# Performance work log

Measured on AMD Instinct MI355X. Metric: run time of the kernel, lower is better.

The kernel has to match this reference:

```python
import jax, jax.numpy as jnp
import numpy as np

EMBED = 1024
HEADS = 16
HEAD_DIM = 64
FF = 4096
EPS = 1e-5


def _layernorm(x, g, b):
    mu = jnp.mean(x, axis=-1, keepdims=True)
    var = jnp.mean(jnp.square(x - mu), axis=-1, keepdims=True)
    return (x - mu) * jax.lax.rsqrt(var + EPS) * g + b


def setup_inputs() -> dict:
    key = jax.random.key(0)
    ks = jax.random.split(key, 12)
    s_in = 1.0 / np.sqrt(EMBED)
    s_hd = 1.0 / np.sqrt(HEADS * HEAD_DIM)
    s_ff = 1.0 / np.sqrt(FF)
    return {
        "x": jax.random.normal(ks[0], (4, 2048, EMBED), dtype=jnp.float32),
        "Wq": jax.random.uniform(ks[1], (HEADS, EMBED, HEAD_DIM), jnp.float32, -s_in, s_in),
        "Wk": jax.random.uniform(ks[2], (HEADS, EMBED, HEAD_DIM), jnp.float32, -s_in, s_in),
        "Wv": jax.random.uniform(ks[3], (HEADS, EMBED, HEAD_DIM), jnp.float32, -s_in, s_in),
        "Wo": jax.random.uniform(ks[4], (HEADS * HEAD_DIM, EMBED), jnp.float32, -s_hd, s_hd),
        "bo": jax.random.uniform(ks[5], (EMBED,), jnp.float32, -s_hd, s_hd),
        "W1": jax.random.uniform(ks[6], (EMBED, FF), jnp.float32, -s_in, s_in),
        "b1": jax.random.uniform(ks[7], (FF,), jnp.float32, -s_in, s_in),
        "W2": jax.random.uniform(ks[8], (FF, EMBED), jnp.float32, -s_ff, s_ff),
        "b2": jax.random.uniform(ks[9], (EMBED,), jnp.float32, -s_ff, s_ff),
        "ln1_g": jnp.ones((EMBED,), jnp.float32),
        "ln1_b": jnp.zeros((EMBED,), jnp.float32),
        "ln2_g": jnp.ones((EMBED,), jnp.float32),
        "ln2_b": jnp.zeros((EMBED,), jnp.float32),
    }


def reference(x, Wq, Wk, Wv, Wo, bo, W1, b1, W2, b2, ln1_g, ln1_b, ln2_g, ln2_b):
    B, T, C = x.shape
    h = _layernorm(x, ln1_g, ln1_b)
    # per-head projections, batched over heads: [B,H,T,Dh]
    q = jnp.einsum("btc,hcd->bhtd", h, Wq)
    k = jnp.einsum("btc,hcd->bhtd", h, Wk)
    v = jnp.einsum("btc,hcd->bhtd", h, Wv)
    scale = HEAD_DIM ** -0.5
    att = jnp.einsum("bhtd,bhsd->bhts", q, k) * scale  # [B,H,T,T]
    causal = jnp.tril(jnp.ones((T, T), dtype=bool))
    att = jnp.where(causal, att, -jnp.inf)
    att = jax.nn.softmax(att, axis=-1)
    out = jnp.einsum("bhts,bhsd->bhtd", att, v)  # [B,H,T,Dh]
    # concat heads (matches torch.cat over head outputs) -> [B,T,H*Dh]
    out = out.transpose(0, 2, 1, 3).reshape(B, T, HEADS * HEAD_DIM)
    x = x + out @ Wo + bo
    h2 = _layernorm(x, ln2_g, ln2_b)
    ff = jax.nn.relu(h2 @ W1 + b1) @ W2 + b2
    return x + ff
```

## Files before the change

kernel.cpp:

```cpp
#include <hip/hip_runtime.h>
#include <hip/hip_bf16.h>

#define EMBED 1024
#define HEADS 16
#define HEAD_DIM 64
#define FFDIM 4096
#define TSEQ 2048
#define BATCH 4
#define ROWS (BATCH * TSEQ)

typedef __bf16 bf16;
typedef __attribute__((ext_vector_type(8))) __bf16 bf16x8;
typedef __attribute__((ext_vector_type(4))) __bf16 bf16x4;
typedef __attribute__((ext_vector_type(4))) float f32x4;
typedef __attribute__((ext_vector_type(16))) float f32x16;
typedef __attribute__((ext_vector_type(2))) unsigned u32x2;

typedef const __attribute__((address_space(1))) void* gvp;
typedef __attribute__((address_space(3))) void* svp;

__device__ inline unsigned pk2(float a, float b) {
  union { bf16 h[2]; unsigned u; } x;
  x.h[0] = (bf16)a;
  x.h[1] = (bf16)b;
  return x.u;
}

__global__ __launch_bounds__(256) void conv_wqkv_t(
    const float* __restrict__ Wq, const float* __restrict__ Wk,
    const float* __restrict__ Wv, bf16* __restrict__ WqkvT) {
  __shared__ bf16 t[64][72];
  int tid = threadIdx.x;
  int k0 = blockIdx.x * 64;
  int head = blockIdx.y;
  int which = blockIdx.z;
  const float* src = which == 0 ? Wq : which == 1 ? Wk : Wv;
  float scale = which == 0 ? 0.125f * 1.44269504088896f : 1.0f;
  src += (size_t)head * 65536;
  bf16* dst = WqkvT + ((size_t)which * 1024 + head * 64) * 1024;
#pragma unroll
  for (int i = 0; i < 4; ++i) {
    int r = i * 16 + (tid >> 4);
    int c = (tid & 15) * 4;
    float4 v = *(const float4*)&src[(size_t)(k0 + r) * 64 + c];
    t[c + 0][r] = (bf16)(v.x * scale);
    t[c + 1][r] = (bf16)(v.y * scale);
    t[c + 2][r] = (bf16)(v.z * scale);
    t[c + 3][r] = (bf16)(v.w * scale);
  }
  __syncthreads();
#pragma unroll
  for (int i = 0; i < 2; ++i) {
    int r = i * 32 + (tid >> 3);
    int c = (tid & 7) * 8;
    bf16x8 o;
#pragma unroll
    for (int j = 0; j < 8; ++j) o[j] = t[r][c + j];
    *(bf16x8*)&dst[(size_t)r * 1024 + k0 + c] = o;
  }
}

__global__ __launch_bounds__(256) void transpose_conv(
    const float* __restrict__ W, bf16* __restrict__ WT, int K, int N) {
  __shared__ bf16 t[64][72];
  int tid = threadIdx.x;
  int n0 = blockIdx.x * 64, k0 = blockIdx.y * 64;
#pragma unroll
  for (int i = 0; i < 4; ++i) {
    int r = i * 16 + (tid >> 4);
    int c = (tid & 15) * 4;
    float4 v = *(const float4*)&W[(size_t)(k0 + r) * N + n0 + c];
    t[c + 0][r] = (bf16)v.x;
    t[c + 1][r] = (bf16)v.y;
    t[c + 2][r] = (bf16)v.z;
    t[c + 3][r] = (bf16)v.w;
  }
  __syncthreads();
#pragma unroll
  for (int i = 0; i < 2; ++i) {
    int r = i * 32 + (tid >> 3);
    int c = (tid & 7) * 8;
    bf16x8 o;
#pragma unroll
    for (int j = 0; j < 8; ++j) o[j] = t[r][c + j];
    *(bf16x8*)&WT[(size_t)(n0 + r) * K + k0 + c] = o;
  }
}

__global__ __launch_bounds__(256) void transpose_v(const bf16* __restrict__ v,
                                                   bf16* __restrict__ vt) {
  __shared__ bf16 t[64][72];
  int bh = blockIdx.y;
  int t0 = blockIdx.x * 64;
  const bf16* src = v + (size_t)bh * 131072;
  bf16* dst = vt + (size_t)bh * 131072;
  int tid = threadIdx.x;
#pragma unroll
  for (int i = 0; i < 2; ++i) {
    int c = tid + i * 256;
    int r = c >> 3, d0 = (c & 7) * 8;
    bf16x8 vv = *(const bf16x8*)&src[(size_t)(t0 + r) * 64 + d0];
#pragma unroll
    for (int j = 0; j < 8; ++j) t[d0 + j][r] = vv[j];
  }
  __syncthreads();
#pragma unroll
  for (int i = 0; i < 2; ++i) {
    int c = tid + i * 256;
    int r = c >> 3, s0 = (c & 7) * 8;
    bf16x8 o;
#pragma unroll
    for (int j = 0; j < 8; ++j) o[j] = t[r][s0 + j];
    *(bf16x8*)&dst[(size_t)r * 2048 + t0 + s0] = o;
  }
}

__global__ __launch_bounds__(256) void ln_kernel(
    const float* __restrict__ x, const float* __restrict__ g,
    const float* __restrict__ bta, bf16* __restrict__ out) {
  int row = blockIdx.x;
  const float* xr = x + (size_t)row * EMBED;
  float4 v = ((const float4*)xr)[threadIdx.x];
  float s1 = v.x + v.y + v.z + v.w;
  float s2 = v.x * v.x + v.y * v.y + v.z * v.z + v.w * v.w;
#pragma unroll
  for (int off = 1; off < 64; off <<= 1) {
    s1 += __shfl_xor(s1, off);
    s2 += __shfl_xor(s2, off);
  }
  __shared__ float red[8];
  int wid = threadIdx.x >> 6;
  int lane = threadIdx.x & 63;
  if (lane == 0) {
    red[wid * 2] = s1;
    red[wid * 2 + 1] = s2;
  }
  __syncthreads();
  s1 = red[0] + red[2] + red[4] + red[6];
  s2 = red[1] + red[3] + red[5] + red[7];
  float mu = s1 * (1.0f / EMBED);
  float var = s2 * (1.0f / EMBED) - mu * mu;
  float rs = rsqrtf(var + 1e-5f);
  float4 gv = ((const float4*)g)[threadIdx.x];
  float4 bv = ((const float4*)bta)[threadIdx.x];
  bf16x4 o;
  o[0] = (bf16)((v.x - mu) * rs * gv.x + bv.x);
  o[1] = (bf16)((v.y - mu) * rs * gv.y + bv.y);
  o[2] = (bf16)((v.z - mu) * rs * gv.z + bv.z);
  o[3] = (bf16)((v.w - mu) * rs * gv.w + bv.w);
  *(bf16x4*)(out + (size_t)row * EMBED + threadIdx.x * 4) = o;
}

template <int EPI>
__global__ __launch_bounds__(512, 1) void gemm256(
    const bf16* __restrict__ A, const bf16* __restrict__ BT,
    bf16* __restrict__ Cb, const float* __restrict__ bias, int M, int N,
    int K) {
  __shared__ __attribute__((aligned(16))) char lds[98304];
  int gx = gridDim.x;
  int nwg = gx * gridDim.y;
  int wgid = blockIdx.y * gx + blockIdx.x;
  int cpx = nwg >> 3;
  int swz = (wgid & 7) * cpx + (wgid >> 3);
  int m0 = (swz / gx) * 256, n0 = (swz % gx) * 256;
  int tid = threadIdx.x;
  int lane = tid & 63, wid = tid >> 6;
  int lr = lane & 15, lg = lane >> 4;
  int wrM = (wid >> 2) * 128;
  int wcN = (wid & 3) * 64;
  int crow = lane >> 2;
  int slotg = (lane & 3) ^ ((crow >> 1) & 3);
  int NT = K >> 5;
  size_t rb = (size_t)K * 2;

  auto stageA = [&](int t) {
    char* dst = lds + ((unsigned)t % 3u) * 32768u;
#pragma unroll
    for (int q = 0; q < 2; ++q) {
      int c = wid * 2 + q;
      const char* srcA = (const char*)A + (size_t)(m0 + c * 16 + crow) * rb +
                         (size_t)t * 64 + slotg * 16;
      __builtin_amdgcn_global_load_lds((gvp)srcA, (svp)(dst + c * 1024), 16, 0,
                                       0);
    }
  };
  auto stageB = [&](int t) {
    char* dst = lds + ((unsigned)t % 3u) * 32768u + 16384u;
#pragma unroll
    for (int q = 0; q < 2; ++q) {
      int c = wid * 2 + q;
      const char* srcB = (const char*)BT + (size_t)(n0 + c * 16 + crow) * rb +
                         (size_t)t * 64 + slotg * 16;
      __builtin_amdgcn_global_load_lds((gvp)srcB, (svp)(dst + c * 1024), 16, 0,
                                       0);
    }
  };

  stageA(0);
  stageB(0);
  stageA(1);
  stageB(1);
  f32x4 acc[8][4] = {};
  int swcol = ((lg ^ ((lr >> 1) & 3)) * 16);
  for (int t = 0; t < NT; ++t) {
    if (t == NT - 1)
      asm volatile("s_waitcnt vmcnt(0)" ::: "memory");
    else
      asm volatile("s_waitcnt vmcnt(4)" ::: "memory");
    __builtin_amdgcn_s_barrier();
    __builtin_amdgcn_sched_barrier(0);
    const char* Ab = lds + ((unsigned)t % 3u) * 32768u;
    const char* Bb = Ab + 16384;
    int tn = t + 2;
    bool st = tn < NT;
    bf16x8 bfr[4], afA[4], afB[4];
#pragma unroll
    for (int j = 0; j < 4; ++j)
      bfr[j] = *(const bf16x8*)(Bb + (wcN + j * 16 + lr) * 64 + swcol);
#pragma unroll
    for (int i = 0; i < 4; ++i)
      afA[i] = *(const bf16x8*)(Ab + (wrM + i * 16 + lr) * 64 + swcol);
    if (st) stageA(tn);
    __builtin_amdgcn_s_barrier();
    __builtin_amdgcn_sched_barrier(0);
    __builtin_amdgcn_s_setprio(1);
#pragma unroll
    for (int i = 0; i < 4; ++i)
#pragma unroll
      for (int j = 0; j < 4; ++j)
        acc[i][j] = __builtin_amdgcn_mfma_f32_16x16x32_bf16(afA[i], bfr[j],
                                                            acc[i][j], 0, 0, 0);
    __builtin_amdgcn_s_setprio(0);
    __builtin_amdgcn_sched_barrier(0);
#pragma unroll
    for (int i = 0; i < 4; ++i)
      afB[i] = *(const bf16x8*)(Ab + (wrM + 64 + i * 16 + lr) * 64 + swcol);
    if (st) stageB(tn);
    __builtin_amdgcn_s_barrier();
    __builtin_amdgcn_sched_barrier(0);
    __builtin_amdgcn_s_setprio(1);
#pragma unroll
    for (int i = 0; i < 4; ++i)
#pragma unroll
      for (int j = 0; j < 4; ++j)
        acc[4 + i][j] = __builtin_amdgcn_mfma_f32_16x16x32_bf16(
            afB[i], bfr[j], acc[4 + i][j], 0, 0, 0);
    __builtin_amdgcn_s_setprio(0);
    __builtin_amdgcn_sched_barrier(0);
  }
#pragma unroll
  for (int i = 0; i < 8; ++i) {
#pragma unroll
    for (int j = 0; j < 4; ++j) {
#pragma unroll
      for (int r = 0; r < 4; ++r) {
        int row = m0 + wrM + i * 16 + lg * 4 + r;
        int col = n0 + wcN + j * 16 + lr;
        float v = acc[i][j][r];
        if (EPI == 0) {
          int which = col >> 10, cc = col & 1023;
          int b = row >> 11, tt = row & 2047, h = cc >> 6, d = cc & 63;
          bf16* dst = Cb + (size_t)which * 8388608;
          dst[((size_t)((b << 4) + h) * TSEQ + tt) * HEAD_DIM + d] = (bf16)v;
        } else {
          size_t o = (size_t)row * N + col;
          float u = v + bias[col];
          Cb[o] = (bf16)(u > 0.f ? u : 0.f);
        }
      }
    }
  }
}

__global__ __launch_bounds__(512, 2) void gemm_res(
    const bf16* __restrict__ A, const bf16* __restrict__ BT,
    float* __restrict__ Cf, const float* __restrict__ bias,
    const float* __restrict__ resid, int M, int N, int K) {
  __shared__ __attribute__((aligned(16))) char lds[73728];
  int gx = gridDim.x;
  int nwg = gx * gridDim.y;
  int wgid = blockIdx.y * gx + blockIdx.x;
  int cpx = nwg >> 3;
  int swz = (wgid & 7) * cpx + (wgid >> 3);
  int m0 = (swz / gx) * 256, n0 = (swz % gx) * 128;
  int tid = threadIdx.x;
  int lane = tid & 63, wid = tid >> 6;
  int lr = lane & 15, lg = lane >> 4;
  int wrM = (wid >> 1) * 64;
  int wcN = (wid & 1) * 64;
  int crow = lane >> 2;
  int slotg = (lane & 3) ^ ((crow >> 1) & 3);
  int NT = K >> 5;
  size_t rb = (size_t)K * 2;

  auto stageA = [&](int t) {
    char* dst = lds + ((unsigned)t % 3u) * 24576u;
#pragma unroll
    for (int q = 0; q < 2; ++q) {
      int c = wid * 2 + q;
      const char* srcA = (const char*)A + (size_t)(m0 + c * 16 + crow) * rb +
                         (size_t)t * 64 + slotg * 16;
      __builtin_amdgcn_global_load_lds((gvp)srcA, (svp)(dst + c * 1024), 16, 0,
                                       0);
    }
  };
  auto stageB = [&](int t) {
    char* dst = lds + ((unsigned)t % 3u) * 24576u + 16384u;
    const char* srcB = (const char*)BT + (size_t)(n0 + wid * 16 + crow) * rb +
                       (size_t)t * 64 + slotg * 16;
    __builtin_amdgcn_global_load_lds((gvp)srcB, (svp)(dst + wid * 1024), 16, 0,
                                     0);
  };

  stageA(0);
  stageB(0);
  stageA(1);
  stageB(1);
  f32x4 acc[4][4] = {};
  int swcol = ((lg ^ ((lr >> 1) & 3)) * 16);
  for (int t = 0; t < NT; ++t) {
    if (t == NT - 1)
      asm volatile("s_waitcnt vmcnt(0)" ::: "memory");
    else
      asm volatile("s_waitcnt vmcnt(3)" ::: "memory");
    __builtin_amdgcn_s_barrier();
    __builtin_amdgcn_sched_barrier(0);
    const char* Ab = lds + ((unsigned)t % 3u) * 24576u;
    const char* Bb = Ab + 16384;
    int tn = t + 2;
    bool st = tn < NT;
    bf16x8 bfr[4], afA[2], afB[2];
#pragma unroll
    for (int j = 0; j < 4; ++j)
      bfr[j] = *(const bf16x8*)(Bb + (wcN + j * 16 + lr) * 64 + swcol);
#pragma unroll
    for (int i = 0; i < 2; ++i)
      afA[i] = *(const bf16x8*)(Ab + (wrM + i * 16 + lr) * 64 + swcol);
    if (st) stageA(tn);
    __builtin_amdgcn_s_barrier();
    __builtin_amdgcn_sched_barrier(0);
    __builtin_amdgcn_s_setprio(1);
#pragma unroll
    for (int i = 0; i < 2; ++i)
#pragma unroll
      for (int j = 0; j < 4; ++j)
        acc[i][j] = __builtin_amdgcn_mfma_f32_16x16x32_bf16(afA[i], bfr[j],
                                                            acc[i][j], 0, 0, 0);
    __builtin_amdgcn_s_setprio(0);
    __builtin_amdgcn_sched_barrier(0);
#pragma unroll
    for (int i = 0; i < 2; ++i)
      afB[i] = *(const bf16x8*)(Ab + (wrM + 32 + i * 16 + lr) * 64 + swcol);
    if (st) stageB(tn);
    __builtin_amdgcn_s_barrier();
    __builtin_amdgcn_sched_barrier(0);
    __builtin_amdgcn_s_setprio(1);
#pragma unroll
    for (int i = 0; i < 2; ++i)
#pragma unroll
      for (int j = 0; j < 4; ++j)
        acc[2 + i][j] = __builtin_amdgcn_mfma_f32_16x16x32_bf16(
            afB[i], bfr[j], acc[2 + i][j], 0, 0, 0);
    __builtin_amdgcn_s_setprio(0);
    __builtin_amdgcn_sched_barrier(0);
  }
#pragma unroll
  for (int i = 0; i < 4; ++i) {
#pragma unroll
    for (int j = 0; j < 4; ++j) {
#pragma unroll
      for (int r = 0; r < 4; ++r) {
        int row = m0 + wrM + i * 16 + lg * 4 + r;
        int col = n0 + wcN + j * 16 + lr;
        size_t o = (size_t)row * N + col;
        Cf[o] = resid[o] + bias[col] + acc[i][j][r];
      }
    }
  }
}

__global__ __launch_bounds__(256) void attn_kernel(
    const bf16* __restrict__ q, const bf16* __restrict__ k,
    const bf16* __restrict__ vt, bf16* __restrict__ out) {
  __shared__ __attribute__((aligned(16))) char ldsK[8192];
  __shared__ __attribute__((aligned(16))) char ldsV[8192];
  int bh = blockIdx.x;
  int b = bh >> 4, h = bh & 15;
  const bf16* qb = q + (size_t)bh * TSEQ * HEAD_DIM;
  const bf16* kb = k + (size_t)bh * TSEQ * HEAD_DIM;
  const bf16* vb = vt + (size_t)bh * HEAD_DIM * TSEQ;
  int tid = threadIdx.x, lane = tid & 63, w = tid >> 6;
  int l31 = lane & 31, hi = lane >> 5;
  int Q = 15 - blockIdx.y;
  int tw = Q * 128 + w * 32;
  int qrow = tw + l31;
  int srow0 = tid >> 3;
  int scol = (tid & 7) * 16;
  int swz31 = (l31 & 7) << 4;
  bf16x8 aq[4];
#pragma unroll
  for (int f = 0; f < 4; ++f)
    aq[f] = *(const bf16x8*)&qb[(size_t)qrow * HEAD_DIM + f * 16 + hi * 8];
  f32x16 o0 = {}, o1 = {};
  f32x16 minit;
#pragma unroll
  for (int i = 0; i < 16; ++i) minit[i] = -8.0f;
  float sacc = 0.f;
  int nj = 2 * Q + 2;
  for (int j = 0; j < nj; ++j) {
#pragma unroll
    for (int i = 0; i < 2; ++i) {
      int rr = srow0 + i * 32;
      int sw = scol ^ ((rr & 7) << 4);
      *(bf16x8*)(ldsK + rr * 128 + sw) =
          *(const bf16x8*)&kb[(size_t)(j * 64 + rr) * HEAD_DIM + (scol >> 1)];
      *(bf16x8*)(ldsV + rr * 128 + sw) =
          *(const bf16x8*)&vb[(size_t)rr * TSEQ + j * 64 + (scol >> 1)];
    }
    __syncthreads();
    if (j * 64 <= tw + 31) {
      f32x16 s0 = minit, s1 = minit;
#pragma unroll
      for (int f = 0; f < 4; ++f) {
        int colb = (f * 32 + hi * 16) ^ swz31;
        bf16x8 ka = *(const bf16x8*)(ldsK + l31 * 128 + colb);
        bf16x8 kb2 = *(const bf16x8*)(ldsK + (32 + l31) * 128 + colb);
        s0 = __builtin_amdgcn_mfma_f32_32x32x16_bf16(ka, aq[f], s0, 0, 0, 0);
        s1 = __builtin_amdgcn_mfma_f32_32x32x16_bf16(kb2, aq[f], s1, 0, 0, 0);
      }
      if (j >= 2 * Q) {
#pragma unroll
        for (int reg = 0; reg < 16; ++reg) {
          int key = j * 64 + (reg & 3) + 8 * (reg >> 2) + 4 * hi;
          if (key > qrow) s0[reg] = -1e30f;
          if (key + 32 > qrow) s1[reg] = -1e30f;
        }
      }
      unsigned pk0[8], pk1[8];
#pragma unroll
      for (int p = 0; p < 8; ++p) {
        float a0 = exp2f(s0[2 * p]), b0 = exp2f(s0[2 * p + 1]);
        float a1 = exp2f(s1[2 * p]), b1 = exp2f(s1[2 * p + 1]);
        sacc += (a0 + b0) + (a1 + b1);
        pk0[p] = pk2(a0, b0);
        pk1[p] = pk2(a1, b1);
      }
#pragma unroll
      for (int ks = 0; ks < 4; ++ks) {
        const unsigned* P = (ks >> 1) ? pk1 : pk0;
        int kp = (ks & 1) * 4;
        union { unsigned u[4]; bf16x8 v; } pa;
#if __has_builtin(__builtin_amdgcn_permlane32_swap)
        u32x2 r02 = __builtin_amdgcn_permlane32_swap(P[kp + 0], P[kp + 2],
                                                     false, false);
        u32x2 r13 = __builtin_amdgcn_permlane32_swap(P[kp + 1], P[kp + 3],
                                                     false, false);
        pa.u[0] = r02.x;
        pa.u[2] = r02.y;
        pa.u[1] = r13.x;
        pa.u[3] = r13.y;
#else
        unsigned x0 = P[kp + 0], x1 = P[kp + 1];
        unsigned x2 = P[kp + 2], x3 = P[kp + 3];
        unsigned y0 = (unsigned)__shfl_xor((int)x0, 32);
        unsigned y1 = (unsigned)__shfl_xor((int)x1, 32);
        unsigned y2 = (unsigned)__shfl_xor((int)x2, 32);
        unsigned y3 = (unsigned)__shfl_xor((int)x3, 32);
        pa.u[0] = hi ? y2 : x0;
        pa.u[1] = hi ? y3 : x1;
        pa.u[2] = hi ? x2 : y0;
        pa.u[3] = hi ? x3 : y1;
#endif
        int colb = (ks * 32 + hi * 16) ^ swz31;
        bf16x8 bv0 = *(const bf16x8*)(ldsV + l31 * 128 + colb);
        bf16x8 bv1 = *(const bf16x8*)(ldsV + (32 + l31) * 128 + colb);
        o0 = __builtin_amdgcn_mfma_f32_32x32x16_bf16(pa.v, bv0, o0, 0, 0, 0);
        o1 = __builtin_amdgcn_mfma_f32_32x32x16_bf16(pa.v, bv1, o1, 0, 0, 0);
      }
    }
    __syncthreads();
  }
  float tot = sacc + __shfl_xor(sacc, 32);
#pragma unroll
  for (int reg = 0; reg < 16; ++reg) {
    int ql = (reg & 3) + 8 * (reg >> 2) + 4 * hi;
    float lw = __shfl(tot, ql);
    float rl = 1.0f / lw;
    int t = tw + ql;
    size_t o = ((size_t)(b * TSEQ) + t) * EMBED + h * HEAD_DIM;
    out[o + l31] = (bf16)(o0[reg] * rl);
    out[o + 32 + l31] = (bf16)(o1[reg] * rl);
  }
}

extern "C" void kernel_launch(void* const* d_in, const int* in_sizes, int n_in,
                              void* d_out, int out_size, void* d_ws,
                              size_t ws_size, hipStream_t stream) {
  const float* x = (const float*)d_in[0];
  const float* Wq = (const float*)d_in[1];
  const float* Wk = (const float*)d_in[2];
  const float* Wv = (const float*)d_in[3];
  const float* Wo = (const float*)d_in[4];
  const float* bo = (const float*)d_in[5];
  const float* W1 = (const float*)d_in[6];
  const float* b1 = (const float*)d_in[7];
  const float* W2 = (const float*)d_in[8];
  const float* b2 = (const float*)d_in[9];
  const float* g1 = (const float*)d_in[10];
  const float* be1 = (const float*)d_in[11];
  const float* g2 = (const float*)d_in[12];
  const float* be2 = (const float*)d_in[13];
  float* out = (float*)d_out;
  char* ws = (char*)d_ws;

  const size_t U = 16777216;
  bf16* h = (bf16*)(ws + 0 * U);
  bf16* qb = (bf16*)(ws + 1 * U);
  bf16* vtb = (bf16*)(ws + 0 * U);
  bf16* vnb = (bf16*)(ws + 3 * U);
  bf16* ao = (bf16*)(ws + 3 * U);
  float* x1 = (float*)(ws + 4 * U);
  bf16* h2 = (bf16*)(ws + 6 * U);
  bf16* ff1 = (bf16*)(ws + 0 * U);
  char* wbase = ws + 7 * U;
  bf16* WqkvT = (bf16*)(wbase);
  bf16* WoT = (bf16*)(wbase + 6291456);
  bf16* W1T = (bf16*)(wbase + 8388608);
  bf16* W2T = (bf16*)(wbase + 16777216);

  hipLaunchKernelGGL(conv_wqkv_t, dim3(16, 16, 3), dim3(256), 0, stream, Wq,
                     Wk, Wv, WqkvT);
  hipLaunchKernelGGL(transpose_conv, dim3(16, 16), dim3(256), 0, stream, Wo,
                     WoT, 1024, 1024);
  hipLaunchKernelGGL(transpose_conv, dim3(64, 16), dim3(256), 0, stream, W1,
                     W1T, 1024, 4096);
  hipLaunchKernelGGL(transpose_conv, dim3(16, 64), dim3(256), 0, stream, W2,
                     W2T, 4096, 1024);
  hipLaunchKernelGGL(ln_kernel, dim3(8192), dim3(256), 0, stream, x, g1, be1,
                     h);
  hipLaunchKernelGGL((gemm256<0>), dim3(12, 32), dim3(512), 0, stream, h,
                     WqkvT, qb, (const float*)nullptr, ROWS, 3072, 1024);
  hipLaunchKernelGGL(transpose_v, dim3(32, 64), dim3(256), 0, stream, vnb,
                     vtb);
  hipLaunchKernelGGL(attn_kernel, dim3(64, 16), dim3(256), 0, stream, qb,
                     qb + 8388608, vtb, ao);
  hipLaunchKernelGGL(gemm_res, dim3(8, 32), dim3(512), 0, stream, ao, WoT, x1,
                     bo, x, ROWS, 1024, 1024);
  hipLaunchKernelGGL(ln_kernel, dim3(8192), dim3(256), 0, stream, x1, g2, be2,
                     h2);
  hipLaunchKernelGGL((gemm256<3>), dim3(16, 32), dim3(512), 0, stream, h2, W1T,
                     ff1, b1, ROWS, 4096, 1024);
  hipLaunchKernelGGL(gemm_res, dim3(8, 32), dim3(512), 0, stream, ff1, W2T,
                     out, b2, x1, ROWS, 1024, 4096);
}
```

Before: 382.1 us.

## Shrink attention blocks to 64 queries to drop masked-tile waste

```diff
diff --git a/kernel.cpp b/kernel.cpp
--- a/kernel.cpp
+++ b/kernel.cpp
@@ -14,7 +14,6 @@
 typedef __attribute__((ext_vector_type(4))) __bf16 bf16x4;
 typedef __attribute__((ext_vector_type(4))) float f32x4;
 typedef __attribute__((ext_vector_type(16))) float f32x16;
-typedef __attribute__((ext_vector_type(2))) unsigned u32x2;
 
 typedef const __attribute__((address_space(1))) void* gvp;
 typedef __attribute__((address_space(3))) void* svp;
@@ -379,7 +378,7 @@
   }
 }
 
-__global__ __launch_bounds__(256) void attn_kernel(
+__global__ __launch_bounds__(128) void attn_kernel(
     const bf16* __restrict__ q, const bf16* __restrict__ k,
     const bf16* __restrict__ vt, bf16* __restrict__ out) {
   __shared__ __attribute__((aligned(16))) char ldsK[8192];
@@ -391,8 +390,8 @@
   const bf16* vb = vt + (size_t)bh * HEAD_DIM * TSEQ;
   int tid = threadIdx.x, lane = tid & 63, w = tid >> 6;
   int l31 = lane & 31, hi = lane >> 5;
-  int Q = 15 - blockIdx.y;
-  int tw = Q * 128 + w * 32;
+  int Q = 31 - blockIdx.y;
+  int tw = Q * 64 + w * 32;
   int qrow = tw + l31;
   int srow0 = tid >> 3;
   int scol = (tid & 7) * 16;
@@ -406,11 +405,11 @@
 #pragma unroll
   for (int i = 0; i < 16; ++i) minit[i] = -8.0f;
   float sacc = 0.f;
-  int nj = 2 * Q + 2;
+  int nj = Q + 1;
   for (int j = 0; j < nj; ++j) {
 #pragma unroll
-    for (int i = 0; i < 2; ++i) {
-      int rr = srow0 + i * 32;
+    for (int i = 0; i < 4; ++i) {
+      int rr = srow0 + i * 16;
       int sw = scol ^ ((rr & 7) << 4);
       *(bf16x8*)(ldsK + rr * 128 + sw) =
           *(const bf16x8*)&kb[(size_t)(j * 64 + rr) * HEAD_DIM + (scol >> 1)];
@@ -418,66 +417,55 @@
           *(const bf16x8*)&vb[(size_t)rr * TSEQ + j * 64 + (scol >> 1)];
     }
     __syncthreads();
-    if (j * 64 <= tw + 31) {
-      f32x16 s0 = minit, s1 = minit;
-#pragma unroll
-      for (int f = 0; f < 4; ++f) {
-        int colb = (f * 32 + hi * 16) ^ swz31;
-        bf16x8 ka = *(const bf16x8*)(ldsK + l31 * 128 + colb);
-        bf16x8 kb2 = *(const bf16x8*)(ldsK + (32 + l31) * 128 + colb);
-        s0 = __builtin_amdgcn_mfma_f32_32x32x16_bf16(ka, aq[f], s0, 0, 0, 0);
-        s1 = __builtin_amdgcn_mfma_f32_32x32x16_bf16(kb2, aq[f], s1, 0, 0, 0);
+    f32x16 s0 = minit, s1 = minit;
+    __builtin_amdgcn_s_setprio(1);
+#pragma unroll
+    for (int f = 0; f < 4; ++f) {
+      int colb = (f * 32 + hi * 16) ^ swz31;
+      bf16x8 ka = *(const bf16x8*)(ldsK + l31 * 128 + colb);
+      bf16x8 kb2 = *(const bf16x8*)(ldsK + (32 + l31) * 128 + colb);
+      s0 = __builtin_amdgcn_mfma_f32_32x32x16_bf16(ka, aq[f], s0, 0, 0, 0);
+      s1 = __builtin_amdgcn_mfma_f32_32x32x16_bf16(kb2, aq[f], s1, 0, 0, 0);
+    }
+    __builtin_amdgcn_s_setprio(0);
+    if (j == Q) {
+#pragma unroll
+      for (int reg = 0; reg < 16; ++reg) {
+        int key = j * 64 + (reg & 3) + 8 * (reg >> 2) + 4 * hi;
+        if (key > qrow) s0[reg] = -1e30f;
+        if (key + 32 > qrow) s1[reg] = -1e30f;
       }
-      if (j >= 2 * Q) {
-#pragma unroll
-        for (int reg = 0; reg < 16; ++reg) {
-          int key = j * 64 + (reg & 3) + 8 * (reg >> 2) + 4 * hi;
-          if (key > qrow) s0[reg] = -1e30f;
-          if (key + 32 > qrow) s1[reg] = -1e30f;
-        }
-      }
-      unsigned pk0[8], pk1[8];
-#pragma unroll
-      for (int p = 0; p < 8; ++p) {
-        float a0 = exp2f(s0[2 * p]), b0 = exp2f(s0[2 * p + 1]);
-        float a1 = exp2f(s1[2 * p]), b1 = exp2f(s1[2 * p + 1]);
-        sacc += (a0 + b0) + (a1 + b1);
-        pk0[p] = pk2(a0, b0);
-        pk1[p] = pk2(a1, b1);
-      }
-#pragma unroll
-      for (int ks = 0; ks < 4; ++ks) {
-        const unsigned* P = (ks >> 1) ? pk1 : pk0;
-        int kp = (ks & 1) * 4;
-        union { unsigned u[4]; bf16x8 v; } pa;
-#if __has_builtin(__builtin_amdgcn_permlane32_swap)
-        u32x2 r02 = __builtin_amdgcn_permlane32_swap(P[kp + 0], P[kp + 2],
-                                                     false, false);
-        u32x2 r13 = __builtin_amdgcn_permlane32_swap(P[kp + 1], P[kp + 3],
-                                                     false, false);
-        pa.u[0] = r02.x;
-        pa.u[2] = r02.y;
-        pa.u[1] = r13.x;
-        pa.u[3] = r13.y;
-#else
-        unsigned x0 = P[kp + 0], x1 = P[kp + 1];
-        unsigned x2 = P[kp + 2], x3 = P[kp + 3];
-        unsigned y0 = (unsigned)__shfl_xor((int)x0, 32);
-        unsigned y1 = (unsigned)__shfl_xor((int)x1, 32);
-        unsigned y2 = (unsigned)__shfl_xor((int)x2, 32);
-        unsigned y3 = (unsigned)__shfl_xor((int)x3, 32);
-        pa.u[0] = hi ? y2 : x0;
-        pa.u[1] = hi ? y3 : x1;
-        pa.u[2] = hi ? x2 : y0;
-        pa.u[3] = hi ? x3 : y1;
-#endif
-        int colb = (ks * 32 + hi * 16) ^ swz31;
-        bf16x8 bv0 = *(const bf16x8*)(ldsV + l31 * 128 + colb);
-        bf16x8 bv1 = *(const bf16x8*)(ldsV + (32 + l31) * 128 + colb);
-        o0 = __builtin_amdgcn_mfma_f32_32x32x16_bf16(pa.v, bv0, o0, 0, 0, 0);
-        o1 = __builtin_amdgcn_mfma_f32_32x32x16_bf16(pa.v, bv1, o1, 0, 0, 0);
-      }
-    }
+    }
+    unsigned pk0[8], pk1[8];
+#pragma unroll
+    for (int p = 0; p < 8; ++p) {
+      float a0 = exp2f(s0[2 * p]), b0 = exp2f(s0[2 * p + 1]);
+      float a1 = exp2f(s1[2 * p]), b1 = exp2f(s1[2 * p + 1]);
+      sacc += (a0 + b0) + (a1 + b1);
+      pk0[p] = pk2(a0, b0);
+      pk1[p] = pk2(a1, b1);
+    }
+    __builtin_amdgcn_s_setprio(1);
+#pragma unroll
+    for (int ks = 0; ks < 4; ++ks) {
+      const unsigned* P = (ks >> 1) ? pk1 : pk0;
+      int kp = (ks & 1) * 4;
+      unsigned x0 = P[kp + 0], x1 = P[kp + 1];
+      unsigned x2 = P[kp + 2], x3 = P[kp + 3];
+      asm("v_permlane32_swap_b32 %0, %1" : "+v"(x0), "+v"(x2));
+      asm("v_permlane32_swap_b32 %0, %1" : "+v"(x1), "+v"(x3));
+      union { unsigned u[4]; bf16x8 v; } pa;
+      pa.u[0] = x0;
+      pa.u[1] = x1;
+      pa.u[2] = x2;
+      pa.u[3] = x3;
+      int colb = (ks * 32 + hi * 16) ^ swz31;
+      bf16x8 bv0 = *(const bf16x8*)(ldsV + l31 * 128 + colb);
+      bf16x8 bv1 = *(const bf16x8*)(ldsV + (32 + l31) * 128 + colb);
+      o0 = __builtin_amdgcn_mfma_f32_32x32x16_bf16(pa.v, bv0, o0, 0, 0, 0);
+      o1 = __builtin_amdgcn_mfma_f32_32x32x16_bf16(pa.v, bv1, o1, 0, 0, 0);
+    }
+    __builtin_amdgcn_s_setprio(0);
     __syncthreads();
   }
   float tot = sacc + __shfl_xor(sacc, 32);
@@ -542,7 +530,7 @@
                      WqkvT, qb, (const float*)nullptr, ROWS, 3072, 1024);
   hipLaunchKernelGGL(transpose_v, dim3(32, 64), dim3(256), 0, stream, vnb,
                      vtb);
-  hipLaunchKernelGGL(attn_kernel, dim3(64, 16), dim3(256), 0, stream, qb,
+  hipLaunchKernelGGL(attn_kernel, dim3(64, 32), dim3(128), 0, stream, qb,
                      qb + 8388608, vtb, ao);
   hipLaunchKernelGGL(gemm_res, dim3(8, 32), dim3(512), 0, stream, ao, WoT, x1,
                      bo, x, ROWS, 1024, 1024);
```

Result: no change. 386.6 us (+1.2%).
